# Kernel tuning notes

Measured on AMD Instinct MI355X. Metric: run time of the kernel, lower is better.

## Reference

```python
import jax, jax.numpy as jnp
import numpy as np

B, N, DIN, DOUT, DOP = 64, 512, 256, 256, 64
LN_EPS = 1e-5
NEG_SLOPE = 0.2


def setup_inputs() -> dict:
    key = jax.random.key(0)
    ks = jax.random.split(key, 16)
    stdv = 1.0 / np.sqrt(DOUT)

    def lin(k, shape, fan_in):
        # torch nn.Linear default init: U(-1/sqrt(fan_in), 1/sqrt(fan_in))
        bound = 1.0 / np.sqrt(fan_in)
        return jax.random.uniform(k, shape, jnp.float32, -bound, bound)

    return {
        "inputs": jax.random.normal(ks[0], (B, N, DIN), jnp.float32),
        "adj": jax.random.uniform(ks[1], (B, N, N), jnp.float32),
        "op_emb": jax.random.normal(ks[2], (B, N, DOP), jnp.float32),
        # DenseGraphFlow params
        "dgf_W": jax.random.uniform(ks[3], (DIN, DOUT), jnp.float32, -stdv, stdv),
        "dgf_b": jax.random.uniform(ks[4], (DOUT,), jnp.float32, -stdv, stdv),
        "dgf_opW": lin(ks[5], (DOUT, DOP), DOP),
        "dgf_opb": lin(ks[6], (DOUT,), DOP),
        # GraphAttentionLayer params
        "Wk": lin(ks[7], (DOUT, DIN), DIN),
        "Wv": lin(ks[8], (DOUT, DIN), DIN),
        "Wq": lin(ks[9], (DOUT, DIN), DIN),
        "a_w": lin(ks[10], (DOUT,), DOUT),
        "gat_opW": lin(ks[11], (DOUT, DOP), DOP),
        "gat_opb": lin(ks[12], (DOUT,), DOP),
        "ln_g": jnp.ones((DOUT,), jnp.float32),
        "ln_b": jnp.zeros((DOUT,), jnp.float32),
    }


def reference(inputs, adj, op_emb, dgf_W, dgf_b, dgf_opW, dgf_opb,
              Wk, Wv, Wq, a_w, gat_opW, gat_opb, ln_g, ln_b):
    # ----- DenseGraphFlow branch -----
    support = jnp.einsum('bni,io->bno', inputs, dgf_W)            # [B,N,DOUT]
    gate_d = jax.nn.sigmoid(op_emb @ dgf_opW.T + dgf_opb)        # [B,N,DOUT]
    dense = gate_d * jnp.einsum('bij,bjo->bio', adj, support)
    dense = dense + support + dgf_b                               # residual + bias

    # ----- GraphAttentionLayer branch -----
    Whk = inputs @ Wk.T                                           # [B,N,DOUT]
    Whv = inputs @ Wv.T
    Whq = inputs @ Wq.T
    # torch einsum 'balm,beam->belm' (a=1) builds Whq[b,e,:]*Whk[b,l,:];
    # a(.) contracts the feature dim -> equivalent fused score:
    scores = jnp.einsum('bem,blm,m->bel', Whq, Whk, a_w)
    scores = scores / jnp.sqrt(jnp.float32(DOUT))                 # attention_rescale
    alpha = jax.nn.leaky_relu(scores, NEG_SLOPE) * adj            # mask by multiply
    attn = jax.nn.softmax(alpha, axis=-1)                         # softmax over l (neighbors)
    gate_g = jax.nn.sigmoid(op_emb @ gat_opW.T + gat_opb)
    h_prime = gate_g * jnp.einsum('bel,blm->bem', attn, Whv)
    # LayerNorm over last dim
    mu = jnp.mean(h_prime, axis=-1, keepdims=True)
    var = jnp.var(h_prime, axis=-1, keepdims=True)
    gat = (h_prime - mu) * jax.lax.rsqrt(var + LN_EPS) * ln_g + ln_b

    return (dense + gat) * 0.5
```

## Files before the change

### kernel.cpp

```cpp
#include <hip/hip_runtime.h>
#include <cstdint>
#include <cstddef>

typedef unsigned short u16;
typedef unsigned int   u32;
typedef __attribute__((ext_vector_type(8))) short bf16x8;
typedef __attribute__((ext_vector_type(4))) float f32x4;

#define MFMA16(a,b,c) __builtin_amdgcn_mfma_f32_16x16x32_bf16((a),(b),(c),0,0,0)

__device__ __forceinline__ float bf2f(u16 h){
  union { u32 u; float f; } v; v.u = ((u32)h) << 16; return v.f;
}
__device__ __forceinline__ u16 f2bf(float f){
  union { float f; u32 u; } v; v.f = f;
  u32 u = v.u + 0x7FFFu + ((v.u >> 16) & 1u);
  return (u16)(u >> 16);
}
__device__ __forceinline__ float ldf(const void* p, int i, u32 isf32){
  return isf32 ? ((const float*)p)[i] : bf2f(((const u16*)p)[i]);
}

__global__ void kD_detect(const u16* __restrict__ raw, u32* __restrict__ flag)
{
  const int lane = threadIdx.x & 63;
  const float v = bf2f(raw[lane]);
  const unsigned long long big = __ballot(fabsf(v) > 1.0e6f);
  if (lane == 0) flag[0] = (big != 0ull) ? 1u : 0u;
}

__global__ void kC_conv(const void* __restrict__ src, u16* __restrict__ dst,
                        int n, const u32* __restrict__ flag)
{
  const int i8 = (blockIdx.x * 256 + threadIdx.x) << 3;
  if (i8 >= n) return;
  if (flag[0]) {
    const float4 a = ((const float4*)src)[i8 >> 2];
    const float4 b = ((const float4*)src)[(i8 >> 2) + 1];
    u16 o[8] = { f2bf(a.x), f2bf(a.y), f2bf(a.z), f2bf(a.w),
                 f2bf(b.x), f2bf(b.y), f2bf(b.z), f2bf(b.w) };
    *(uint4*)&dst[i8] = *(const uint4*)o;
  } else {
    ((uint4*)dst)[i8 >> 3] = ((const uint4*)src)[i8 >> 3];
  }
}

__global__ void kP_params(const void* dgf_opW, const void* gat_opW,
                          const void* dgf_b,   const void* dgf_opb,
                          const void* gat_opb, const void* ln_g,
                          const void* ln_b,    u16* __restrict__ PB,
                          const u32* __restrict__ flag)
{
  const int i = blockIdx.x * 256 + threadIdx.x;
  if (i >= 34048) return;
  const u32 f = flag[0];
  float v;
  if      (i < 16384) v = ldf(dgf_opW, i, f);
  else if (i < 32768) v = ldf(gat_opW, i - 16384, f);
  else if (i < 33024) v = ldf(dgf_b,   i - 32768, f);
  else if (i < 33280) v = ldf(dgf_opb, i - 33024, f);
  else if (i < 33536) v = ldf(gat_opb, i - 33280, f);
  else if (i < 33792) v = ldf(ln_g,    i - 33536, f);
  else                v = ldf(ln_b,    i - 33792, f);
  PB[i] = f2bf(v);
}

__global__ void k0_wcat(const void* dgfW, const void* Wk, const void* Wv,
                        const void* Wq, const void* aw, u16* __restrict__ Wcat,
                        const u32* __restrict__ flag)
{
  const int o = blockIdx.x;
  const int i = threadIdx.x;
  const u32 f = flag[0];
  float v;
  if (o < 256)       v = ldf(dgfW, i * 256 + o, f);
  else if (o < 512)  v = ldf(Wk, (o - 256) * 256 + i, f);
  else if (o < 768)  v = ldf(Wv, (o - 512) * 256 + i, f);
  else               v = ldf(Wq, (o - 768) * 256 + i, f) * ldf(aw, o - 768, f) * 0.0625f;
  Wcat[o * 256 + i] = f2bf(v);
}

__global__ __launch_bounds__(256, 2)
void k1_proj(const u16* __restrict__ X, const u16* __restrict__ W,
             u16* __restrict__ P, u16* __restrict__ T)
{
  __shared__ __align__(16) u16 ldsA[128 * 64];
  __shared__ __align__(16) u16 ldsB[128 * 64];
  const int bt = blockIdx.x;
  const int ct = blockIdx.y;
  const int r0 = bt << 7;
  const bool swapped = (ct == 4) | (ct == 5) | (ct >= 8);
  const int wbase = (ct < 8) ? (ct << 7) : ((ct - 8) << 7);
  const int tid = threadIdx.x;
  const int wave = tid >> 6;
  const int lane = tid & 63;
  const int wm = wave >> 1, wn = wave & 1;

  f32x4 acc[4][4];
#pragma unroll
  for (int i = 0; i < 4; ++i)
#pragma unroll
    for (int j = 0; j < 4; ++j) acc[i][j] = f32x4{0.f, 0.f, 0.f, 0.f};

  for (int kt = 0; kt < 4; ++kt) {
    __syncthreads();
#pragma unroll
    for (int s = 0; s < 4; ++s) {
      const int slot = ((wave * 4 + s) << 6) + lane;
      const int m = slot >> 3, c = slot & 7;
      const int kb = c ^ (m & 7);
      *(uint4*)&ldsA[slot << 3] =
          *(const uint4*)(X + (r0 + m) * 256 + (kt << 6) + (kb << 3));
      *(uint4*)&ldsB[slot << 3] =
          *(const uint4*)(W + (wbase + m) * 256 + (kt << 6) + (kb << 3));
    }
    __syncthreads();
#pragma unroll
    for (int ks = 0; ks < 2; ++ks) {
      const int kb = (ks << 2) + (lane >> 4);
      bf16x8 fa[4], fb[4];
#pragma unroll
      for (int i = 0; i < 4; ++i) {
        const int m = (wm << 6) + (i << 4) + (lane & 15);
        fa[i] = *(const bf16x8*)&ldsA[((m << 3) + (kb ^ (m & 7))) << 3];
        const int n = (wn << 6) + (i << 4) + (lane & 15);
        fb[i] = *(const bf16x8*)&ldsB[((n << 3) + (kb ^ (n & 7))) << 3];
      }
      if (!swapped) {
#pragma unroll
        for (int i = 0; i < 4; ++i)
#pragma unroll
          for (int j = 0; j < 4; ++j)
            acc[i][j] = MFMA16(fa[i], fb[j], acc[i][j]);
      } else {
#pragma unroll
        for (int i = 0; i < 4; ++i)
#pragma unroll
          for (int j = 0; j < 4; ++j)
            acc[i][j] = MFMA16(fb[i], fa[j], acc[i][j]);
      }
    }
  }

  if (!swapped) {
    const int pcb = (ct < 4) ? (ct << 7) : ((ct - 2) << 7);
#pragma unroll
    for (int i = 0; i < 4; ++i) {
      const int row = r0 + (wm << 6) + (i << 4) + ((lane >> 4) << 2);
#pragma unroll
      for (int j = 0; j < 4; ++j) {
        const int col = pcb + (wn << 6) + (j << 4) + (lane & 15);
#pragma unroll
        for (int r = 0; r < 4; ++r)
          P[(row + r) * 768 + col] = f2bf(acc[i][j][r]);
      }
    }
  } else {
    const int trb = (wbase >= 512) ? (wbase - 256) : wbase;
    const int b = r0 >> 9;
    const int e0 = r0 & 511;
    u16* Tb = T + ((size_t)b << 18);
#pragma unroll
    for (int i = 0; i < 4; ++i) {
      const int trow = trb + (wn << 6) + (i << 4) + ((lane >> 4) << 2);
#pragma unroll
      for (int j = 0; j < 4; ++j) {
        const int e = e0 + (wm << 6) + (j << 4) + (lane & 15);
#pragma unroll
        for (int r = 0; r < 4; ++r)
          Tb[((trow + r) << 9) + e] = f2bf(acc[i][j][r]);
      }
    }
  }
}

__global__ __launch_bounds__(256, 2)
void k2_gates(const u16* __restrict__ OP, const u16* __restrict__ PB,
              u16* __restrict__ G)
{
  __shared__ __align__(16) u16 ldsA[128 * 64];
  __shared__ __align__(16) u16 ldsB[128 * 64];
  const int bt = blockIdx.x, ct = blockIdx.y;
  const int r0 = bt << 7;
  const u16* Wp = (ct < 2) ? (PB + (ct << 7) * 64) : (PB + 16384 + ((ct - 2) << 7) * 64);
  const u16* Bp = (ct < 2) ? (PB + 33024 + (ct << 7)) : (PB + 33280 + ((ct - 2) << 7));
  const int tid = threadIdx.x, wave = tid >> 6, lane = tid & 63;
  const int wm = wave >> 1, wn = wave & 1;

  f32x4 acc[4][4];
#pragma unroll
  for (int i = 0; i < 4; ++i)
#pragma unroll
    for (int j = 0; j < 4; ++j) acc[i][j] = f32x4{0.f, 0.f, 0.f, 0.f};

#pragma unroll
  for (int s = 0; s < 4; ++s) {
    const int slot = ((wave * 4 + s) << 6) + lane;
    const int m = slot >> 3, c = slot & 7;
    const int kb = c ^ (m & 7);
    *(uint4*)&ldsA[slot << 3] = *(const uint4*)(OP + (r0 + m) * 64 + (kb << 3));
    *(uint4*)&ldsB[slot << 3] = *(const uint4*)(Wp + m * 64 + (kb << 3));
  }
  __syncthreads();
#pragma unroll
  for (int ks = 0; ks < 2; ++ks) {
    const int kb = (ks << 2) + (lane >> 4);
    bf16x8 fa[4], fb[4];
#pragma unroll
    for (int i = 0; i < 4; ++i) {
      const int m = (wm << 6) + (i << 4) + (lane & 15);
      fa[i] = *(const bf16x8*)&ldsA[((m << 3) + (kb ^ (m & 7))) << 3];
      const int n = (wn << 6) + (i << 4) + (lane & 15);
      fb[i] = *(const bf16x8*)&ldsB[((n << 3) + (kb ^ (n & 7))) << 3];
    }
#pragma unroll
    for (int i = 0; i < 4; ++i)
#pragma unroll
      for (int j = 0; j < 4; ++j)
        acc[i][j] = MFMA16(fa[i], fb[j], acc[i][j]);
  }
#pragma unroll
  for (int i = 0; i < 4; ++i) {
    const int row = r0 + (wm << 6) + (i << 4) + ((lane >> 4) << 2);
#pragma unroll
    for (int j = 0; j < 4; ++j) {
      const int cw = (wn << 6) + (j << 4) + (lane & 15);
      const float bias = bf2f(Bp[cw]);
      const int col = (ct << 7) + cw;
#pragma unroll
      for (int r = 0; r < 4; ++r) {
        const float x = acc[i][j][r] + bias;
        G[((row + r) << 9) + col] = f2bf(1.0f / (1.0f + __expf(-x)));
      }
    }
  }
}

__global__ __launch_bounds__(256, 2)
void k3_scores(const u16* __restrict__ P, const u16* __restrict__ adj,
               u16* __restrict__ E)
{
  __shared__ __align__(16) u16 ldsA[128 * 64];
  __shared__ __align__(16) u16 ldsB[128 * 64];
  const int lt = blockIdx.x, et = blockIdx.y, b = blockIdx.z;
  const int e0 = et << 7, l0 = lt << 7;
  const int tid = threadIdx.x, wave = tid >> 6, lane = tid & 63;
  const int wm = wave >> 1, wn = wave & 1;
  const int rowQ = (b << 9) + e0;
  const int rowK = (b << 9) + l0;

  f32x4 acc[4][4];
#pragma unroll
  for (int i = 0; i < 4; ++i)
#pragma unroll
    for (int j = 0; j < 4; ++j) acc[i][j] = f32x4{0.f, 0.f, 0.f, 0.f};

  for (int kt = 0; kt < 4; ++kt) {
    __syncthreads();
#pragma unroll
    for (int s = 0; s < 4; ++s) {
      const int slot = ((wave * 4 + s) << 6) + lane;
      const int m = slot >> 3, c = slot & 7;
      const int kb = c ^ (m & 7);
      *(uint4*)&ldsA[slot << 3] =
          *(const uint4*)(P + (rowQ + m) * 768 + 512 + (kt << 6) + (kb << 3));
      *(uint4*)&ldsB[slot << 3] =
          *(const uint4*)(P + (rowK + m) * 768 + 256 + (kt << 6) + (kb << 3));
    }
    __syncthreads();
#pragma unroll
    for (int ks = 0; ks < 2; ++ks) {
      const int kb = (ks << 2) + (lane >> 4);
      bf16x8 fa[4], fb[4];
#pragma unroll
      for (int i = 0; i < 4; ++i) {
        const int m = (wm << 6) + (i << 4) + (lane & 15);
        fa[i] = *(const bf16x8*)&ldsA[((m << 3) + (kb ^ (m & 7))) << 3];
        const int n = (wn << 6) + (i << 4) + (lane & 15);
        fb[i] = *(const bf16x8*)&ldsB[((n << 3) + (kb ^ (n & 7))) << 3];
      }
#pragma unroll
      for (int i = 0; i < 4; ++i)
#pragma unroll
        for (int j = 0; j < 4; ++j)
          acc[i][j] = MFMA16(fa[i], fb[j], acc[i][j]);
    }
  }
#pragma unroll
  for (int i = 0; i < 4; ++i) {
    const int e = e0 + (wm << 6) + (i << 4) + ((lane >> 4) << 2);
#pragma unroll
    for (int j = 0; j < 4; ++j) {
      const int l = l0 + (wn << 6) + (j << 4) + (lane & 15);
#pragma unroll
      for (int r = 0; r < 4; ++r) {
        const int idx = (((b << 9) + e + r) << 9) + l;
        const float a = bf2f(adj[idx]);
        float s = acc[i][j][r];
        s = (s > 0.0f ? s : 0.2f * s) * a;
        E[idx] = f2bf(__expf(s));
      }
    }
  }
}

__global__ void k3b_rowsum(const u16* __restrict__ E, float* __restrict__ S)
{
  const int row = (blockIdx.x << 2) + (threadIdx.x >> 6);
  const int lane = threadIdx.x & 63;
  const uint4 v = *(const uint4*)(const void*)(E + ((size_t)row << 9) + (lane << 3));
  float s = 0.0f;
  const u32 w[4] = {v.x, v.y, v.z, v.w};
#pragma unroll
  for (int q = 0; q < 4; ++q)
    s += bf2f((u16)(w[q] & 0xFFFFu)) + bf2f((u16)(w[q] >> 16));
#pragma unroll
  for (int m = 32; m >= 1; m >>= 1) s += __shfl_xor(s, m, 64);
  if (lane == 0) S[row] = s;
}

__global__ __launch_bounds__(256, 2)
void k4_out(const u16* __restrict__ P, const u16* __restrict__ T,
            const u16* __restrict__ E, const u16* __restrict__ adj,
            const float* __restrict__ S, const u16* __restrict__ G,
            const u16* __restrict__ PB, void* __restrict__ out,
            const u32* __restrict__ flag)
{
  __shared__ __align__(16) u16 ldsA[64 * 64];
  __shared__ __align__(16) u16 ldsB[256 * 64];
  __shared__ float red[64][4];
  const int et = blockIdx.x, b = blockIdx.y;
  const int e0 = et << 6;
  const int tid = threadIdx.x, wave = tid >> 6, lane = tid & 63;
  const int wm = wave >> 1, wn = wave & 1;
  const size_t abase = ((size_t)((b << 9) + e0)) << 9;
  const u16* Ea  = E + abase;
  const u16* Aa  = adj + abase;
  const u16* Tb  = T + ((size_t)b << 18);
  const u16* WhvT = Tb + (256 << 9);
  const u16* SupT = Tb;
  const u16* dgf_b = PB + 32768;
  const u16* ln_g  = PB + 33536;
  const u16* ln_b  = PB + 33792;
  const u32 isf32 = flag[0];

  f32x4 acc[2][2][8];
#pragma unroll
  for (int p = 0; p < 2; ++p)
#pragma unroll
    for (int i = 0; i < 2; ++i)
#pragma unroll
      for (int j = 0; j < 8; ++j) acc[p][i][j] = f32x4{0.f, 0.f, 0.f, 0.f};

#pragma unroll
  for (int ph = 0; ph < 2; ++ph) {
    const u16* Ag = ph ? Aa : Ea;
    const u16* Bg = ph ? SupT : WhvT;
    for (int lt = 0; lt < 8; ++lt) {
      __syncthreads();
#pragma unroll
      for (int s2 = 0; s2 < 2; ++s2) {
        const int slot = ((wave * 2 + s2) << 6) + lane;
        const int m = slot >> 3, c = slot & 7;
        const int kb = c ^ (m & 7);
        *(uint4*)&ldsA[slot << 3] =
            *(const uint4*)(Ag + (m << 9) + (lt << 6) + (kb << 3));
      }
#pragma unroll
      for (int s2 = 0; s2 < 8; ++s2) {
        const int slot = ((wave * 8 + s2) << 6) + lane;
        const int m = slot >> 3, c = slot & 7;
        const int kb = c ^ (m & 7);
        *(uint4*)&ldsB[slot << 3] =
            *(const uint4*)(Bg + (m << 9) + (lt << 6) + (kb << 3));
      }
      __syncthreads();
#pragma unroll
      for (int ks = 0; ks < 2; ++ks) {
        const int kb = (ks << 2) + (lane >> 4);
        bf16x8 fa[2];
#pragma unroll
        for (int i = 0; i < 2; ++i) {
          const int m = (wm << 5) + (i << 4) + (lane & 15);
          fa[i] = *(const bf16x8*)&ldsA[((m << 3) + (kb ^ (m & 7))) << 3];
        }
#pragma unroll
        for (int j = 0; j < 8; ++j) {
          const int n = (wn << 7) + (j << 4) + (lane & 15);
          const bf16x8 fb = *(const bf16x8*)&ldsB[((n << 3) + (kb ^ (n & 7))) << 3];
          acc[ph][0][j] = MFMA16(fa[0], fb, acc[ph][0][j]);
          acc[ph][1][j] = MFMA16(fa[1], fb, acc[ph][1][j]);
        }
      }
    }
  }

  const int cb = wn << 7;
  float lng[8], lnb[8], dgb[8];
#pragma unroll
  for (int j = 0; j < 8; ++j) {
    const int col = cb + (j << 4) + (lane & 15);
    lng[j] = bf2f(ln_g[col]);
    lnb[j] = bf2f(ln_b[col]);
    dgb[j] = bf2f(dgf_b[col]);
  }
#pragma unroll
  for (int i = 0; i < 2; ++i) {
#pragma unroll
    for (int r = 0; r < 4; ++r) {
      const int rl = (wm << 5) + (i << 4) + ((lane >> 4) << 2) + r;
      const int grow = (b << 9) + e0 + rl;
      const float invS = 1.0f / S[grow];
      float ps = 0.0f, pq = 0.0f;
#pragma unroll
      for (int j = 0; j < 8; ++j) {
        const int col = cb + (j << 4) + (lane & 15);
        const float gg = bf2f(G[((size_t)grow << 9) + 256 + col]);
        const float hp = gg * acc[0][i][j][r] * invS;
        acc[0][i][j][r] = hp;
        ps += hp; pq += hp * hp;
      }
#pragma unroll
      for (int m = 1; m < 16; m <<= 1) {
        ps += __shfl_xor(ps, m, 64);
        pq += __shfl_xor(pq, m, 64);
      }
      if ((lane & 15) == 0) { red[rl][wn << 1] = ps; red[rl][(wn << 1) + 1] = pq; }
    }
  }
  __syncthreads();
#pragma unroll
  for (int i = 0; i < 2; ++i) {
#pragma unroll
    for (int r = 0; r < 4; ++r) {
      const int rl = (wm << 5) + (i << 4) + ((lane >> 4) << 2) + r;
      const int grow = (b << 9) + e0 + rl;
      const float mean = (red[rl][0] + red[rl][2]) * (1.0f / 256.0f);
      const float ex2  = (red[rl][1] + red[rl][3]) * (1.0f / 256.0f);
      const float rstd = rsqrtf(ex2 - mean * mean + 1e-5f);
#pragma unroll
      for (int j = 0; j < 8; ++j) {
        const int col = cb + (j << 4) + (lane & 15);
        const float gat = (acc[0][i][j][r] - mean) * rstd * lng[j] + lnb[j];
        const float gd = bf2f(G[((size_t)grow << 9) + col]);
        const float sup = bf2f(P[grow * 768 + col]);
        const float dense = gd * acc[1][i][j][r] + sup + dgb[j];
        const float o = 0.5f * (dense + gat);
        if (isf32) ((float*)out)[grow * 256 + col] = o;
        else       ((u16*)out)[grow * 256 + col] = f2bf(o);
      }
    }
  }
}

extern "C" void kernel_launch(void* const* d_in, const int* in_sizes, int n_in,
                              void* d_out, int out_size, void* d_ws, size_t ws_size,
                              hipStream_t stream)
{
  (void)in_sizes; (void)n_in; (void)out_size; (void)ws_size;
  const void* inputs  = d_in[0];
  const void* adj     = d_in[1];
  const void* op_emb  = d_in[2];
  const void* dgf_W   = d_in[3];
  const void* dgf_b   = d_in[4];
  const void* dgf_opW = d_in[5];
  const void* dgf_opb = d_in[6];
  const void* Wk      = d_in[7];
  const void* Wv      = d_in[8];
  const void* Wq      = d_in[9];
  const void* a_w     = d_in[10];
  const void* gat_opW = d_in[11];
  const void* gat_opb = d_in[12];
  const void* ln_g    = d_in[13];
  const void* ln_b    = d_in[14];
  char* ws = (char*)d_ws;

  u16*  P    = (u16*)(ws);
  u16*  T    = (u16*)(ws + 50331648ull);
  u16*  E    = (u16*)(ws + 83886080ull);
  u16*  G    = (u16*)(ws + 117440512ull);
  u16*  Cadj = (u16*)(ws + 150994944ull);
  u16*  Cin  = (u16*)(ws + 184549376ull);
  u16*  Cop  = (u16*)(ws + 201326592ull);
  u16*  Wcat = (u16*)(ws + 205520896ull);
  u16*  PB   = (u16*)(ws + 206045184ull);
  float* Srw = (float*)(ws + 206114816ull);
  u32*  flag = (u32*)(ws + 206245888ull);

  kD_detect <<<dim3(1),       dim3(64),  0, stream>>>((const u16*)inputs, flag);
  kC_conv   <<<dim3(4096),    dim3(256), 0, stream>>>(inputs, Cin,  8388608, flag);
  kC_conv   <<<dim3(1024),    dim3(256), 0, stream>>>(op_emb, Cop,  2097152, flag);
  kC_conv   <<<dim3(8192),    dim3(256), 0, stream>>>(adj,    Cadj, 16777216, flag);
  kP_params <<<dim3(134),     dim3(256), 0, stream>>>(dgf_opW, gat_opW, dgf_b,
                                                      dgf_opb, gat_opb, ln_g, ln_b,
                                                      PB, flag);
  k0_wcat   <<<dim3(1024),    dim3(256), 0, stream>>>(dgf_W, Wk, Wv, Wq, a_w,
                                                      Wcat, flag);
  k1_proj   <<<dim3(256, 10), dim3(256), 0, stream>>>(Cin, Wcat, P, T);
  k2_gates  <<<dim3(256, 4),  dim3(256), 0, stream>>>(Cop, PB, G);
  k3_scores <<<dim3(4, 4, 64),dim3(256), 0, stream>>>(P, Cadj, E);
  k3b_rowsum<<<dim3(8192),    dim3(256), 0, stream>>>(E, Srw);
  k4_out    <<<dim3(8, 64),   dim3(256), 0, stream>>>(P, T, E, Cadj, Srw, G,
                                                      PB, d_out, flag);
}
```

Before: 334.0 us.

## Fuse prep kernels, fold adj conversion and rowsum into scores, use direct LDS loads

Merges the dtype-detect, input/op_emb conversion, weight concat and parameter packing kernels into one prep kernel that also zeroes the row-sum buffer. The adj conversion pass and the separate row-sum kernel are folded into the scores kernel, which reads raw adj, writes both the converted copy and exp scores, and accumulates row sums with atomics. All GEMM tile loads switch to global_load_lds direct-to-LDS transfers. Launch bounds rise to 4 blocks per CU, and the output kernel halves its row tile to double the grid. The changes cut launches and a full extra pass over adj and E, at the cost of atomics and possible register pressure under the tighter launch bounds.

Measured after the change: 505.0 us. +51.2%, slower.

```diff
diff --git a/kernel.cpp b/kernel.cpp
--- a/kernel.cpp
+++ b/kernel.cpp
@@ -20,21 +20,17 @@
 __device__ __forceinline__ float ldf(const void* p, int i, u32 isf32){
   return isf32 ? ((const float*)p)[i] : bf2f(((const u16*)p)[i]);
 }
-
-__global__ void kD_detect(const u16* __restrict__ raw, u32* __restrict__ flag)
-{
-  const int lane = threadIdx.x & 63;
-  const float v = bf2f(raw[lane]);
-  const unsigned long long big = __ballot(fabsf(v) > 1.0e6f);
-  if (lane == 0) flag[0] = (big != 0ull) ? 1u : 0u;
-}
-
-__global__ void kC_conv(const void* __restrict__ src, u16* __restrict__ dst,
-                        int n, const u32* __restrict__ flag)
-{
-  const int i8 = (blockIdx.x * 256 + threadIdx.x) << 3;
-  if (i8 >= n) return;
-  if (flag[0]) {
+__device__ __forceinline__ u32 detectf32(const void* p){
+  const float v = bf2f(((const u16*)p)[threadIdx.x & 63]);
+  return (__ballot(fabsf(v) > 1.0e6f) != 0ull) ? 1u : 0u;
+}
+__device__ __forceinline__ void gload_lds16(const u16* g, u16* lbase){
+  auto gp = (const __attribute__((address_space(1))) u32*)(uintptr_t)g;
+  auto lp = (__attribute__((address_space(3))) u32*)(uintptr_t)lbase;
+  __builtin_amdgcn_global_load_lds(gp, lp, 16, 0, 0);
+}
+__device__ __forceinline__ void conv8(const void* src, u16* dst, int i8, u32 f){
+  if (f) {
     const float4 a = ((const float4*)src)[i8 >> 2];
     const float4 b = ((const float4*)src)[(i8 >> 2) + 1];
     u16 o[8] = { f2bf(a.x), f2bf(a.y), f2bf(a.z), f2bf(a.w),
@@ -45,42 +41,49 @@
   }
 }
 
-__global__ void kP_params(const void* dgf_opW, const void* gat_opW,
-                          const void* dgf_b,   const void* dgf_opb,
-                          const void* gat_opb, const void* ln_g,
-                          const void* ln_b,    u16* __restrict__ PB,
-                          const u32* __restrict__ flag)
-{
-  const int i = blockIdx.x * 256 + threadIdx.x;
-  if (i >= 34048) return;
-  const u32 f = flag[0];
-  float v;
-  if      (i < 16384) v = ldf(dgf_opW, i, f);
-  else if (i < 32768) v = ldf(gat_opW, i - 16384, f);
-  else if (i < 33024) v = ldf(dgf_b,   i - 32768, f);
-  else if (i < 33280) v = ldf(dgf_opb, i - 33024, f);
-  else if (i < 33536) v = ldf(gat_opb, i - 33280, f);
-  else if (i < 33792) v = ldf(ln_g,    i - 33536, f);
-  else                v = ldf(ln_b,    i - 33792, f);
-  PB[i] = f2bf(v);
-}
-
-__global__ void k0_wcat(const void* dgfW, const void* Wk, const void* Wv,
-                        const void* Wq, const void* aw, u16* __restrict__ Wcat,
-                        const u32* __restrict__ flag)
-{
-  const int o = blockIdx.x;
-  const int i = threadIdx.x;
-  const u32 f = flag[0];
-  float v;
-  if (o < 256)       v = ldf(dgfW, i * 256 + o, f);
-  else if (o < 512)  v = ldf(Wk, (o - 256) * 256 + i, f);
-  else if (o < 768)  v = ldf(Wv, (o - 512) * 256 + i, f);
-  else               v = ldf(Wq, (o - 768) * 256 + i, f) * ldf(aw, o - 768, f) * 0.0625f;
-  Wcat[o * 256 + i] = f2bf(v);
-}
-
-__global__ __launch_bounds__(256, 2)
+__global__ void kPrep(const void* inputs, const void* op_emb,
+                      const void* dgfW, const void* Wk, const void* Wv,
+                      const void* Wq, const void* aw,
+                      const void* dgf_opW, const void* gat_opW,
+                      const void* dgf_b, const void* dgf_opb,
+                      const void* gat_opb, const void* ln_g, const void* ln_b,
+                      u16* __restrict__ Cin, u16* __restrict__ Cop,
+                      u16* __restrict__ Wcat, u16* __restrict__ PB,
+                      float* __restrict__ Srw)
+{
+  const u32 f = detectf32(inputs);
+  const int bid = blockIdx.x, tid = threadIdx.x;
+  if (bid < 4096) {
+    conv8(inputs, Cin, ((bid << 8) + tid) << 3, f);
+  } else if (bid < 5120) {
+    conv8(op_emb, Cop, (((bid - 4096) << 8) + tid) << 3, f);
+  } else if (bid < 6144) {
+    const int o = bid - 5120, i = tid;
+    float v;
+    if (o < 256)       v = ldf(dgfW, i * 256 + o, f);
+    else if (o < 512)  v = ldf(Wk, (o - 256) * 256 + i, f);
+    else if (o < 768)  v = ldf(Wv, (o - 512) * 256 + i, f);
+    else               v = ldf(Wq, (o - 768) * 256 + i, f) * ldf(aw, o - 768, f) * 0.0625f;
+    Wcat[o * 256 + i] = f2bf(v);
+  } else if (bid < 6278) {
+    const int i = ((bid - 6144) << 8) + tid;
+    if (i < 34048) {
+      float v;
+      if      (i < 16384) v = ldf(dgf_opW, i, f);
+      else if (i < 32768) v = ldf(gat_opW, i - 16384, f);
+      else if (i < 33024) v = ldf(dgf_b,   i - 32768, f);
+      else if (i < 33280) v = ldf(dgf_opb, i - 33024, f);
+      else if (i < 33536) v = ldf(gat_opb, i - 33280, f);
+      else if (i < 33792) v = ldf(ln_g,    i - 33536, f);
+      else                v = ldf(ln_b,    i - 33792, f);
+      PB[i] = f2bf(v);
+    }
+  } else {
+    ((float4*)Srw)[((bid - 6278) << 8) + tid] = float4{0.f, 0.f, 0.f, 0.f};
+  }
+}
+
+__global__ __launch_bounds__(256, 4)
 void k1_proj(const u16* __restrict__ X, const u16* __restrict__ W,
              u16* __restrict__ P, u16* __restrict__ T)
 {
@@ -106,13 +109,12 @@
     __syncthreads();
 #pragma unroll
     for (int s = 0; s < 4; ++s) {
-      const int slot = ((wave * 4 + s) << 6) + lane;
+      const int bslot = (wave * 4 + s) << 6;
+      const int slot = bslot + lane;
       const int m = slot >> 3, c = slot & 7;
       const int kb = c ^ (m & 7);
-      *(uint4*)&ldsA[slot << 3] =
-          *(const uint4*)(X + (r0 + m) * 256 + (kt << 6) + (kb << 3));
-      *(uint4*)&ldsB[slot << 3] =
-          *(const uint4*)(W + (wbase + m) * 256 + (kt << 6) + (kb << 3));
+      gload_lds16(X + (r0 + m) * 256 + (kt << 6) + (kb << 3), &ldsA[bslot << 3]);
+      gload_lds16(W + (wbase + m) * 256 + (kt << 6) + (kb << 3), &ldsB[bslot << 3]);
     }
     __syncthreads();
 #pragma unroll
@@ -174,7 +176,7 @@
   }
 }
 
-__global__ __launch_bounds__(256, 2)
+__global__ __launch_bounds__(256, 4)
 void k2_gates(const u16* __restrict__ OP, const u16* __restrict__ PB,
               u16* __restrict__ G)
 {
@@ -195,11 +197,12 @@
 
 #pragma unroll
   for (int s = 0; s < 4; ++s) {
-    const int slot = ((wave * 4 + s) << 6) + lane;
+    const int bslot = (wave * 4 + s) << 6;
+    const int slot = bslot + lane;
     const int m = slot >> 3, c = slot & 7;
     const int kb = c ^ (m & 7);
-    *(uint4*)&ldsA[slot << 3] = *(const uint4*)(OP + (r0 + m) * 64 + (kb << 3));
-    *(uint4*)&ldsB[slot << 3] = *(const uint4*)(Wp + m * 64 + (kb << 3));
+    gload_lds16(OP + (r0 + m) * 64 + (kb << 3), &ldsA[bslot << 3]);
+    gload_lds16(Wp + m * 64 + (kb << 3), &ldsB[bslot << 3]);
   }
   __syncthreads();
 #pragma unroll
@@ -236,9 +239,10 @@
   }
 }
 
-__global__ __launch_bounds__(256, 2)
-void k3_scores(const u16* __restrict__ P, const u16* __restrict__ adj,
-               u16* __restrict__ E)
+__global__ __launch_bounds__(256, 4)
+void k3_scores(const u16* __restrict__ P, const void* __restrict__ adjR,
+               u16* __restrict__ E, u16* __restrict__ Cadj,
+               float* __restrict__ Srw)
 {
   __shared__ __align__(16) u16 ldsA[128 * 64];
   __shared__ __align__(16) u16 ldsB[128 * 64];
@@ -248,6 +252,7 @@
   const int wm = wave >> 1, wn = wave & 1;
   const int rowQ = (b << 9) + e0;
   const int rowK = (b << 9) + l0;
+  const u32 isf32 = detectf32(adjR);
 
   f32x4 acc[4][4];
 #pragma unroll
@@ -259,13 +264,12 @@
     __syncthreads();
 #pragma unroll
     for (int s = 0; s < 4; ++s) {
-      const int slot = ((wave * 4 + s) << 6) + lane;
+      const int bslot = (wave * 4 + s) << 6;
+      const int slot = bslot + lane;
       const int m = slot >> 3, c = slot & 7;
       const int kb = c ^ (m & 7);
-      *(uint4*)&ldsA[slot << 3] =
-          *(const uint4*)(P + (rowQ + m) * 768 + 512 + (kt << 6) + (kb << 3));
-      *(uint4*)&ldsB[slot << 3] =
-          *(const uint4*)(P + (rowK + m) * 768 + 256 + (kt << 6) + (kb << 3));
+      gload_lds16(P + (rowQ + m) * 768 + 512 + (kt << 6) + (kb << 3), &ldsA[bslot << 3]);
+      gload_lds16(P + (rowK + m) * 768 + 256 + (kt << 6) + (kb << 3), &ldsB[bslot << 3]);
     }
     __syncthreads();
 #pragma unroll
@@ -288,69 +292,61 @@
   }
 #pragma unroll
   for (int i = 0; i < 4; ++i) {
-    const int e = e0 + (wm << 6) + (i << 4) + ((lane >> 4) << 2);
-#pragma unroll
-    for (int j = 0; j < 4; ++j) {
-      const int l = l0 + (wn << 6) + (j << 4) + (lane & 15);
-#pragma unroll
-      for (int r = 0; r < 4; ++r) {
-        const int idx = (((b << 9) + e + r) << 9) + l;
-        const float a = bf2f(adj[idx]);
+#pragma unroll
+    for (int r = 0; r < 4; ++r) {
+      const int e = e0 + (wm << 6) + (i << 4) + ((lane >> 4) << 2) + r;
+      const int grow = (b << 9) + e;
+      float part = 0.0f;
+#pragma unroll
+      for (int j = 0; j < 4; ++j) {
+        const int l = l0 + (wn << 6) + (j << 4) + (lane & 15);
+        const int idx = (grow << 9) + l;
+        const float a = isf32 ? ((const float*)adjR)[idx]
+                              : bf2f(((const u16*)adjR)[idx]);
         float s = acc[i][j][r];
         s = (s > 0.0f ? s : 0.2f * s) * a;
-        E[idx] = f2bf(__expf(s));
-      }
-    }
-  }
-}
-
-__global__ void k3b_rowsum(const u16* __restrict__ E, float* __restrict__ S)
-{
-  const int row = (blockIdx.x << 2) + (threadIdx.x >> 6);
-  const int lane = threadIdx.x & 63;
-  const uint4 v = *(const uint4*)(const void*)(E + ((size_t)row << 9) + (lane << 3));
-  float s = 0.0f;
-  const u32 w[4] = {v.x, v.y, v.z, v.w};
-#pragma unroll
-  for (int q = 0; q < 4; ++q)
-    s += bf2f((u16)(w[q] & 0xFFFFu)) + bf2f((u16)(w[q] >> 16));
-#pragma unroll
-  for (int m = 32; m >= 1; m >>= 1) s += __shfl_xor(s, m, 64);
-  if (lane == 0) S[row] = s;
-}
-
-__global__ __launch_bounds__(256, 2)
+        const float ex = __expf(s);
+        E[idx] = f2bf(ex);
+        Cadj[idx] = f2bf(a);
+        part += ex;
+      }
+#pragma unroll
+      for (int m = 1; m < 16; m <<= 1) part += __shfl_xor(part, m, 64);
+      if ((lane & 15) == 0) atomicAdd(&Srw[grow], part);
+    }
+  }
+}
+
+__global__ __launch_bounds__(256, 4)
 void k4_out(const u16* __restrict__ P, const u16* __restrict__ T,
-            const u16* __restrict__ E, const u16* __restrict__ adj,
+            const u16* __restrict__ E, const u16* __restrict__ Cadj,
             const float* __restrict__ S, const u16* __restrict__ G,
             const u16* __restrict__ PB, void* __restrict__ out,
-            const u32* __restrict__ flag)
-{
-  __shared__ __align__(16) u16 ldsA[64 * 64];
+            const void* __restrict__ rawIn)
+{
+  __shared__ __align__(16) u16 ldsA[32 * 64];
   __shared__ __align__(16) u16 ldsB[256 * 64];
-  __shared__ float red[64][4];
+  __shared__ float red[32][4];
   const int et = blockIdx.x, b = blockIdx.y;
-  const int e0 = et << 6;
+  const int e0 = et << 5;
   const int tid = threadIdx.x, wave = tid >> 6, lane = tid & 63;
   const int wm = wave >> 1, wn = wave & 1;
   const size_t abase = ((size_t)((b << 9) + e0)) << 9;
   const u16* Ea  = E + abase;
-  const u16* Aa  = adj + abase;
+  const u16* Aa  = Cadj + abase;
   const u16* Tb  = T + ((size_t)b << 18);
   const u16* WhvT = Tb + (256 << 9);
   const u16* SupT = Tb;
   const u16* dgf_b = PB + 32768;
   const u16* ln_g  = PB + 33536;
   const u16* ln_b  = PB + 33792;
-  const u32 isf32 = flag[0];
-
-  f32x4 acc[2][2][8];
+  const u32 isf32 = detectf32(rawIn);
+
+  f32x4 acc[2][8];
 #pragma unroll
   for (int p = 0; p < 2; ++p)
 #pragma unroll
-    for (int i = 0; i < 2; ++i)
-#pragma unroll
-      for (int j = 0; j < 8; ++j) acc[p][i][j] = f32x4{0.f, 0.f, 0.f, 0.f};
+    for (int j = 0; j < 8; ++j) acc[p][j] = f32x4{0.f, 0.f, 0.f, 0.f};
 
 #pragma unroll
   for (int ph = 0; ph < 2; ++ph) {
@@ -358,38 +354,32 @@
     const u16* Bg = ph ? SupT : WhvT;
     for (int lt = 0; lt < 8; ++lt) {
       __syncthreads();
-#pragma unroll
-      for (int s2 = 0; s2 < 2; ++s2) {
-        const int slot = ((wave * 2 + s2) << 6) + lane;
+      {
+        const int bslot = wave << 6;
+        const int slot = bslot + lane;
         const int m = slot >> 3, c = slot & 7;
         const int kb = c ^ (m & 7);
-        *(uint4*)&ldsA[slot << 3] =
-            *(const uint4*)(Ag + (m << 9) + (lt << 6) + (kb << 3));
+        gload_lds16(Ag + (m << 9) + (lt << 6) + (kb << 3), &ldsA[bslot << 3]);
       }
 #pragma unroll
       for (int s2 = 0; s2 < 8; ++s2) {
-        const int slot = ((wave * 8 + s2) << 6) + lane;
+        const int bslot = (wave * 8 + s2) << 6;
+        const int slot = bslot + lane;
         const int m = slot >> 3, c = slot & 7;
         const int kb = c ^ (m & 7);
-        *(uint4*)&ldsB[slot << 3] =
-            *(const uint4*)(Bg + (m << 9) + (lt << 6) + (kb << 3));
+        gload_lds16(Bg + (m << 9) + (lt << 6) + (kb << 3), &ldsB[bslot << 3]);
       }
       __syncthreads();
 #pragma unroll
       for (int ks = 0; ks < 2; ++ks) {
         const int kb = (ks << 2) + (lane >> 4);
-        bf16x8 fa[2];
-#pragma unroll
-        for (int i = 0; i < 2; ++i) {
-          const int m = (wm << 5) + (i << 4) + (lane & 15);
-          fa[i] = *(const bf16x8*)&ldsA[((m << 3) + (kb ^ (m & 7))) << 3];
-        }
+        const int m = (wm << 4) + (lane & 15);
+        const bf16x8 fa = *(const bf16x8*)&ldsA[((m << 3) + (kb ^ (m & 7))) << 3];
 #pragma unroll
         for (int j = 0; j < 8; ++j) {
           const int n = (wn << 7) + (j << 4) + (lane & 15);
           const bf16x8 fb = *(const bf16x8*)&ldsB[((n << 3) + (kb ^ (n & 7))) << 3];
-          acc[ph][0][j] = MFMA16(fa[0], fb, acc[ph][0][j]);
-          acc[ph][1][j] = MFMA16(fa[1], fb, acc[ph][1][j]);
+          acc[ph][j] = MFMA16(fa, fb, acc[ph][j]);
         }
       }
     }
@@ -405,50 +395,44 @@
     dgb[j] = bf2f(dgf_b[col]);
   }
 #pragma unroll
-  for (int i = 0; i < 2; ++i) {
-#pragma unroll
-    for (int r = 0; r < 4; ++r) {
-      const int rl = (wm << 5) + (i << 4) + ((lane >> 4) << 2) + r;
-      const int grow = (b << 9) + e0 + rl;
-      const float invS = 1.0f / S[grow];
-      float ps = 0.0f, pq = 0.0f;
-#pragma unroll
-      for (int j = 0; j < 8; ++j) {
-        const int col = cb + (j << 4) + (lane & 15);
-        const float gg = bf2f(G[((size_t)grow << 9) + 256 + col]);
-        const float hp = gg * acc[0][i][j][r] * invS;
-        acc[0][i][j][r] = hp;
-        ps += hp; pq += hp * hp;
-      }
-#pragma unroll
-      for (int m = 1; m < 16; m <<= 1) {
-        ps += __shfl_xor(ps, m, 64);
-        pq += __shfl_xor(pq, m, 64);
-      }
-      if ((lane & 15) == 0) { red[rl][wn << 1] = ps; red[rl][(wn << 1) + 1] = pq; }
-    }
+  for (int r = 0; r < 4; ++r) {
+    const int rl = (wm << 4) + ((lane >> 4) << 2) + r;
+    const int grow = (b << 9) + e0 + rl;
+    const float invS = 1.0f / S[grow];
+    float ps = 0.0f, pq = 0.0f;
+#pragma unroll
+    for (int j = 0; j < 8; ++j) {
+      const int col = cb + (j << 4) + (lane & 15);
+      const float gg = bf2f(G[((size_t)grow << 9) + 256 + col]);
+      const float hp = gg * acc[0][j][r] * invS;
+      acc[0][j][r] = hp;
+      ps += hp; pq += hp * hp;
+    }
+#pragma unroll
+    for (int m = 1; m < 16; m <<= 1) {
+      ps += __shfl_xor(ps, m, 64);
+      pq += __shfl_xor(pq, m, 64);
+    }
+    if ((lane & 15) == 0) { red[rl][wn << 1] = ps; red[rl][(wn << 1) + 1] = pq; }
   }
   __syncthreads();
 #pragma unroll
-  for (int i = 0; i < 2; ++i) {
-#pragma unroll
-    for (int r = 0; r < 4; ++r) {
-      const int rl = (wm << 5) + (i << 4) + ((lane >> 4) << 2) + r;
-      const int grow = (b << 9) + e0 + rl;
-      const float mean = (red[rl][0] + red[rl][2]) * (1.0f / 256.0f);
-      const float ex2  = (red[rl][1] + red[rl][3]) * (1.0f / 256.0f);
-      const float rstd = rsqrtf(ex2 - mean * mean + 1e-5f);
-#pragma unroll
-      for (int j = 0; j < 8; ++j) {
-        const int col = cb + (j << 4) + (lane & 15);
-        const float gat = (acc[0][i][j][r] - mean) * rstd * lng[j] + lnb[j];
-        const float gd = bf2f(G[((size_t)grow << 9) + col]);
-        const float sup = bf2f(P[grow * 768 + col]);
-        const float dense = gd * acc[1][i][j][r] + sup + dgb[j];
-        const float o = 0.5f * (dense + gat);
-        if (isf32) ((float*)out)[grow * 256 + col] = o;
-        else       ((u16*)out)[grow * 256 + col] = f2bf(o);
-      }
+  for (int r = 0; r < 4; ++r) {
+    const int rl = (wm << 4) + ((lane >> 4) << 2) + r;
+    const int grow = (b << 9) + e0 + rl;
+    const float mean = (red[rl][0] + red[rl][2]) * (1.0f / 256.0f);
+    const float ex2  = (red[rl][1] + red[rl][3]) * (1.0f / 256.0f);
+    const float rstd = rsqrtf(ex2 - mean * mean + 1e-5f);
+#pragma unroll
+    for (int j = 0; j < 8; ++j) {
+      const int col = cb + (j << 4) + (lane & 15);
+      const float gat = (acc[0][j][r] - mean) * rstd * lng[j] + lnb[j];
+      const float gd = bf2f(G[((size_t)grow << 9) + col]);
+      const float sup = bf2f(P[grow * 768 + col]);
+      const float dense = gd * acc[1][j][r] + sup + dgb[j];
+      const float o = 0.5f * (dense + gat);
+      if (isf32) ((float*)out)[grow * 256 + col] = o;
+      else       ((u16*)out)[grow * 256 + col] = f2bf(o);
     }
   }
 }
@@ -485,21 +469,13 @@
   u16*  Wcat = (u16*)(ws + 205520896ull);
   u16*  PB   = (u16*)(ws + 206045184ull);
   float* Srw = (float*)(ws + 206114816ull);
-  u32*  flag = (u32*)(ws + 206245888ull);
-
-  kD_detect <<<dim3(1),       dim3(64),  0, stream>>>((const u16*)inputs, flag);
-  kC_conv   <<<dim3(4096),    dim3(256), 0, stream>>>(inputs, Cin,  8388608, flag);
-  kC_conv   <<<dim3(1024),    dim3(256), 0, stream>>>(op_emb, Cop,  2097152, flag);
-  kC_conv   <<<dim3(8192),    dim3(256), 0, stream>>>(adj,    Cadj, 16777216, flag);
-  kP_params <<<dim3(134),     dim3(256), 0, stream>>>(dgf_opW, gat_opW, dgf_b,
-                                                      dgf_opb, gat_opb, ln_g, ln_b,
-                                                      PB, flag);
-  k0_wcat   <<<dim3(1024),    dim3(256), 0, stream>>>(dgf_W, Wk, Wv, Wq, a_w,
-                                                      Wcat, flag);
-  k1_proj   <<<dim3(256, 10), dim3(256), 0, stream>>>(Cin, Wcat, P, T);
-  k2_gates  <<<dim3(256, 4),  dim3(256), 0, stream>>>(Cop, PB, G);
-  k3_scores <<<dim3(4, 4, 64),dim3(256), 0, stream>>>(P, Cadj, E);
-  k3b_rowsum<<<dim3(8192),    dim3(256), 0, stream>>>(E, Srw);
-  k4_out    <<<dim3(8, 64),   dim3(256), 0, stream>>>(P, T, E, Cadj, Srw, G,
-                                                      PB, d_out, flag);
-}
+
+  kPrep    <<<dim3(6310),     dim3(256), 0, stream>>>(inputs, op_emb,
+                dgf_W, Wk, Wv, Wq, a_w, dgf_opW, gat_opW, dgf_b, dgf_opb,
+                gat_opb, ln_g, ln_b, Cin, Cop, Wcat, PB, Srw);
+  k1_proj  <<<dim3(256, 10),  dim3(256), 0, stream>>>(Cin, Wcat, P, T);
+  k2_gates <<<dim3(256, 4),   dim3(256), 0, stream>>>(Cop, PB, G);
+  k3_scores<<<dim3(4, 4, 64), dim3(256), 0, stream>>>(P, adj, E, Cadj, Srw);
+  k4_out   <<<dim3(16, 64),   dim3(256), 0, stream>>>(P, T, E, Cadj, Srw, G,
+                                                      PB, d_out, inputs);
+}
```
